# Kernel tuning notes

Measured on AMD Instinct MI355X. Metric: run time of the kernel, lower is better.

## Reference

```python
import jax, jax.numpy as jnp
import numpy as np

WINDOW = 5
PAD = WINDOW // 2


def _extract_patches(x):
    # x: (B,C,H,W) -> patches (B,C,K*K,H,W) with reflect padding, matching
    # F.pad(mode='reflect') + F.unfold(window, padding=0).
    B, C, H, W = x.shape
    xp = jnp.pad(x, ((0, 0), (0, 0), (PAD, PAD), (PAD, PAD)), mode='reflect')
    patches = jnp.stack(
        [xp[:, :, i:i + H, j:j + W] for i in range(WINDOW) for j in range(WINDOW)],
        axis=2,
    )
    return patches


def setup_inputs() -> dict:
    key = jax.random.key(0)
    k1, k2, k3 = jax.random.split(key, 3)
    x = jax.random.normal(k1, (4, 32, 256, 256), dtype=jnp.float32)
    mix = jax.random.normal(k2, (1, 32, 1, 1), dtype=jnp.float32)
    beta_raw = jax.random.normal(k3, (), dtype=jnp.float32)
    return {"x": x, "mix": mix, "beta_raw": beta_raw}


def reference(x, mix, beta_raw):
    patches = _extract_patches(x)  # (B,C,25,H,W)

    # Max filter (= max_pool2d over reflect-padded input, stride 1)
    max_out = jnp.max(patches, axis=2)

    # Soft (differentiable) median filter
    beta = 5.0 + 45.0 * jax.nn.sigmoid(beta_raw)
    center = jnp.mean(patches, axis=2, keepdims=True)
    weights = jax.nn.softmax(-beta * jnp.abs(patches - center), axis=2)
    median_out = jnp.sum(weights * patches, axis=2)

    lambda_c = jax.nn.sigmoid(mix)  # (1,C,1,1)
    return lambda_c * median_out + (1.0 - lambda_c) * max_out
```

## Files before the change

kernel.cpp:

```cpp
#include <hip/hip_runtime.h>
#include <math.h>

#define HW 256
#define TW 128
#define TH 32
#define LW 132
#define LH 36

__device__ __forceinline__ int reflect_idx(int i) {
    i = (i < 0) ? -i : i;
    i = (i >= HW) ? (2 * HW - 2 - i) : i;
    return i;
}

__device__ __forceinline__ float4 max4(float4 a, float4 b) {
    float4 r; r.x = fmaxf(a.x, b.x); r.y = fmaxf(a.y, b.y);
    r.z = fmaxf(a.z, b.z); r.w = fmaxf(a.w, b.w); return r;
}
__device__ __forceinline__ float4 add4(float4 a, float4 b) {
    float4 r; r.x = a.x + b.x; r.y = a.y + b.y;
    r.z = a.z + b.z; r.w = a.w + b.w; return r;
}
__device__ __forceinline__ float4 sub4(float4 a, float4 b) {
    float4 r; r.x = a.x - b.x; r.y = a.y - b.y;
    r.z = a.z - b.z; r.w = a.w - b.w; return r;
}

#define PROC_ROW(A0,B0,A1,B1,A2,B2,A3,B3,A4,B4, OUTROW)                         \
  do {                                                                          \
    const float4 cmA = max4(max4(max4(A0,A1), max4(A2,A3)), A4);                \
    const float4 cmB = max4(max4(max4(B0,B1), max4(B2,B3)), B4);                \
    const float csv[8] = {csA.x,csA.y,csA.z,csA.w, csB.x,csB.y,csB.z,csB.w};    \
    const float cmv[8] = {cmA.x,cmA.y,cmA.z,cmA.w, cmB.x,cmB.y,cmB.z,cmB.w};    \
    const float vv[5][8] = {                                                    \
      {A0.x,A0.y,A0.z,A0.w, B0.x,B0.y,B0.z,B0.w},                               \
      {A1.x,A1.y,A1.z,A1.w, B1.x,B1.y,B1.z,B1.w},                               \
      {A2.x,A2.y,A2.z,A2.w, B2.x,B2.y,B2.z,B2.w},                               \
      {A3.x,A3.y,A3.z,A3.w, B3.x,B3.y,B3.z,B3.w},                               \
      {A4.x,A4.y,A4.z,A4.w, B4.x,B4.y,B4.z,B4.w}};                              \
    float o[4];                                                                 \
    _Pragma("unroll")                                                           \
    for (int p = 0; p < 4; ++p) {                                               \
      const float sum  = csv[p]+csv[p+1]+csv[p+2]+csv[p+3]+csv[p+4];            \
      const float mean = sum * 0.04f;                                           \
      const float m = fmaxf(fmaxf(fmaxf(cmv[p],cmv[p+1]),                       \
                                  fmaxf(cmv[p+2],cmv[p+3])), cmv[p+4]);         \
      float wsum = 0.0f, wacc = 0.0f;                                           \
      _Pragma("unroll")                                                         \
      for (int k = 0; k < 5; ++k) {                                             \
        _Pragma("unroll")                                                       \
        for (int j = 0; j < 5; ++j) {                                           \
          const float d = vv[k][p+j] - mean;                                    \
          const float e = __builtin_amdgcn_exp2f(fabsf(d) * nbl2e);             \
          wsum += e;                                                            \
          wacc = fmaf(e, d, wacc);                                              \
        }                                                                       \
      }                                                                         \
      const float med = fmaf(wacc, __builtin_amdgcn_rcpf(wsum), mean);          \
      o[p] = fmaf(lam, med - m, m);                                             \
    }                                                                           \
    float4 o4; o4.x = o[0]; o4.y = o[1]; o4.z = o[2]; o4.w = o[3];              \
    *(float4*)(orow + (size_t)(OUTROW) * HW) = o4;                              \
  } while (0)

__global__ __launch_bounds__(256, 4)
void maxmedian_kernel(const float* __restrict__ x,
                      const float* __restrict__ mix,
                      const float* __restrict__ beta_raw,
                      float* __restrict__ out,
                      int C) {
    __shared__ __align__(16) float tile[LH * LW];

    const int tiles_x = HW / TW;
    const int tiles_per_plane = tiles_x * (HW / TH);
    const int plane = blockIdx.x / tiles_per_plane;
    const int t     = blockIdx.x % tiles_per_plane;
    const int ty0 = (t / tiles_x) * TH;
    const int tx0 = (t % tiles_x) * TW;

    const float* __restrict__ xp = x + (size_t)plane * (HW * HW);
    const int tid = threadIdx.x;

    {
        const int c  = tid & 127;
        const int r0 = tid >> 7;
        const int gx = tx0 + c;
        #pragma unroll
        for (int k = 0; k < 18; ++k) {
            const int r  = r0 + 2 * k;
            const int gy = reflect_idx(ty0 + r - 2);
            tile[r * LW + (c + 2)] = xp[gy * HW + gx];
        }
        if (tid < 144) {
            const int jj = tid & 3;
            const int j  = (jj < 2) ? jj : (128 + jj);
            const int r  = tid >> 2;
            const int gx2 = reflect_idx(tx0 + j - 2);
            const int gy2 = reflect_idx(ty0 + r - 2);
            tile[r * LW + j] = xp[gy2 * HW + gx2];
        }
    }
    __syncthreads();

    const int ch = plane % C;
    const float lam  = 1.0f / (1.0f + __expf(-mix[ch]));
    const float beta = 5.0f + 45.0f / (1.0f + __expf(-beta_raw[0]));
    const float nbl2e = -beta * 1.44269504088896f;

    const int tx  = tid & 31;
    const int tyq = tid >> 5;
    const int r0 = tyq * 4;

    const float* lbase = &tile[r0 * LW + 4 * tx];

    float4 w0a = *(const float4*)(lbase + 0 * LW);
    float4 w0b = *(const float4*)(lbase + 0 * LW + 4);
    float4 w1a = *(const float4*)(lbase + 1 * LW);
    float4 w1b = *(const float4*)(lbase + 1 * LW + 4);
    float4 w2a = *(const float4*)(lbase + 2 * LW);
    float4 w2b = *(const float4*)(lbase + 2 * LW + 4);
    float4 w3a = *(const float4*)(lbase + 3 * LW);
    float4 w3b = *(const float4*)(lbase + 3 * LW + 4);
    float4 w4a = *(const float4*)(lbase + 4 * LW);
    float4 w4b = *(const float4*)(lbase + 4 * LW + 4);

    float4 csA = add4(add4(add4(w0a, w1a), add4(w2a, w3a)), w4a);
    float4 csB = add4(add4(add4(w0b, w1b), add4(w2b, w3b)), w4b);

    float* __restrict__ orow =
        out + (size_t)plane * (HW * HW) + (size_t)(ty0 + r0) * HW + (tx0 + 4 * tx);

    PROC_ROW(w0a,w0b, w1a,w1b, w2a,w2b, w3a,w3b, w4a,w4b, 0);
    {
        const float4 na = *(const float4*)(lbase + 5 * LW);
        const float4 nb = *(const float4*)(lbase + 5 * LW + 4);
        csA = add4(csA, sub4(na, w0a));
        csB = add4(csB, sub4(nb, w0b));
        w0a = na; w0b = nb;
    }
    PROC_ROW(w1a,w1b, w2a,w2b, w3a,w3b, w4a,w4b, w0a,w0b, 1);
    {
        const float4 na = *(const float4*)(lbase + 6 * LW);
        const float4 nb = *(const float4*)(lbase + 6 * LW + 4);
        csA = add4(csA, sub4(na, w1a));
        csB = add4(csB, sub4(nb, w1b));
        w1a = na; w1b = nb;
    }
    PROC_ROW(w2a,w2b, w3a,w3b, w4a,w4b, w0a,w0b, w1a,w1b, 2);
    {
        const float4 na = *(const float4*)(lbase + 7 * LW);
        const float4 nb = *(const float4*)(lbase + 7 * LW + 4);
        csA = add4(csA, sub4(na, w2a));
        csB = add4(csB, sub4(nb, w2b));
        w2a = na; w2b = nb;
    }
    PROC_ROW(w3a,w3b, w4a,w4b, w0a,w0b, w1a,w1b, w2a,w2b, 3);
}

extern "C" void kernel_launch(void* const* d_in, const int* in_sizes, int n_in,
                              void* d_out, int out_size, void* d_ws, size_t ws_size,
                              hipStream_t stream) {
    const float* x        = (const float*)d_in[0];
    const float* mix      = (const float*)d_in[1];
    const float* beta_raw = (const float*)d_in[2];
    float* out            = (float*)d_out;

    const int planes = in_sizes[0] / (HW * HW);
    const int C      = in_sizes[1];
    const int tiles_per_plane = (HW / TW) * (HW / TH);
    const int grid = planes * tiles_per_plane;

    maxmedian_kernel<<<grid, 256, 0, stream>>>(x, mix, beta_raw, out, C);
}
```

Measured before the change: 45.78 us.

## Halve tile width, process two rows per thread, and pre-scale exp arguments by beta

Tile width drops from 128 to 64, so there are twice as many blocks, and each thread now computes 2 output rows instead of 4. The per-pixel math pre-multiplies by beta*log2e, which turns each exp argument into a single fma followed by a negated abs. Horizontal window sums and maxes share partial sums across the 4 pixels, and vertical column maxes are shared between the two rows. The aim is more parallelism and fewer ALU ops per exp, at the cost of more halo overhead per output and less vertical reuse of the sliding window.

After: 39.57 us. 13.6% less time.

```diff
diff --git a/kernel.cpp b/kernel.cpp
--- a/kernel.cpp
+++ b/kernel.cpp
@@ -2,9 +2,9 @@
 #include <math.h>
 
 #define HW 256
-#define TW 128
+#define TW 64
 #define TH 32
-#define LW 132
+#define LW 68
 #define LH 36
 
 __device__ __forceinline__ int reflect_idx(int i) {
@@ -17,6 +17,10 @@
     float4 r; r.x = fmaxf(a.x, b.x); r.y = fmaxf(a.y, b.y);
     r.z = fmaxf(a.z, b.z); r.w = fmaxf(a.w, b.w); return r;
 }
+__device__ __forceinline__ float4 max34(float4 a, float4 b, float4 c) {
+    float4 r; r.x = fmaxf(fmaxf(a.x, b.x), c.x); r.y = fmaxf(fmaxf(a.y, b.y), c.y);
+    r.z = fmaxf(fmaxf(a.z, b.z), c.z); r.w = fmaxf(fmaxf(a.w, b.w), c.w); return r;
+}
 __device__ __forceinline__ float4 add4(float4 a, float4 b) {
     float4 r; r.x = a.x + b.x; r.y = a.y + b.y;
     r.z = a.z + b.z; r.w = a.w + b.w; return r;
@@ -26,42 +30,66 @@
     r.z = a.z - b.z; r.w = a.w - b.w; return r;
 }
 
-#define PROC_ROW(A0,B0,A1,B1,A2,B2,A3,B3,A4,B4, OUTROW)                         \
-  do {                                                                          \
-    const float4 cmA = max4(max4(max4(A0,A1), max4(A2,A3)), A4);                \
-    const float4 cmB = max4(max4(max4(B0,B1), max4(B2,B3)), B4);                \
-    const float csv[8] = {csA.x,csA.y,csA.z,csA.w, csB.x,csB.y,csB.z,csB.w};    \
-    const float cmv[8] = {cmA.x,cmA.y,cmA.z,cmA.w, cmB.x,cmB.y,cmB.z,cmB.w};    \
-    const float vv[5][8] = {                                                    \
-      {A0.x,A0.y,A0.z,A0.w, B0.x,B0.y,B0.z,B0.w},                               \
-      {A1.x,A1.y,A1.z,A1.w, B1.x,B1.y,B1.z,B1.w},                               \
-      {A2.x,A2.y,A2.z,A2.w, B2.x,B2.y,B2.z,B2.w},                               \
-      {A3.x,A3.y,A3.z,A3.w, B3.x,B3.y,B3.z,B3.w},                               \
-      {A4.x,A4.y,A4.z,A4.w, B4.x,B4.y,B4.z,B4.w}};                              \
-    float o[4];                                                                 \
-    _Pragma("unroll")                                                           \
-    for (int p = 0; p < 4; ++p) {                                               \
-      const float sum  = csv[p]+csv[p+1]+csv[p+2]+csv[p+3]+csv[p+4];            \
-      const float mean = sum * 0.04f;                                           \
-      const float m = fmaxf(fmaxf(fmaxf(cmv[p],cmv[p+1]),                       \
-                                  fmaxf(cmv[p+2],cmv[p+3])), cmv[p+4]);         \
-      float wsum = 0.0f, wacc = 0.0f;                                           \
-      _Pragma("unroll")                                                         \
-      for (int k = 0; k < 5; ++k) {                                             \
-        _Pragma("unroll")                                                       \
-        for (int j = 0; j < 5; ++j) {                                           \
-          const float d = vv[k][p+j] - mean;                                    \
-          const float e = __builtin_amdgcn_exp2f(fabsf(d) * nbl2e);             \
-          wsum += e;                                                            \
-          wacc = fmaf(e, d, wacc);                                              \
-        }                                                                       \
-      }                                                                         \
-      const float med = fmaf(wacc, __builtin_amdgcn_rcpf(wsum), mean);          \
-      o[p] = fmaf(lam, med - m, m);                                             \
-    }                                                                           \
-    float4 o4; o4.x = o[0]; o4.y = o[1]; o4.z = o[2]; o4.w = o[3];              \
-    *(float4*)(orow + (size_t)(OUTROW) * HW) = o4;                              \
-  } while (0)
+__device__ __forceinline__ void proc_row(
+    float4 A0, float4 B0, float4 A1, float4 B1, float4 A2, float4 B2,
+    float4 A3, float4 B3, float4 A4, float4 B4,
+    float4 cmA, float4 cmB, float4 csA, float4 csB,
+    float bp, float c04b, float inv_bp, float lam,
+    float* __restrict__ orow)
+{
+    const float cs[8] = {csA.x,csA.y,csA.z,csA.w, csB.x,csB.y,csB.z,csB.w};
+    const float cm[8] = {cmA.x,cmA.y,cmA.z,cmA.w, cmB.x,cmB.y,cmB.z,cmB.w};
+    const float vv[5][8] = {
+        {A0.x,A0.y,A0.z,A0.w, B0.x,B0.y,B0.z,B0.w},
+        {A1.x,A1.y,A1.z,A1.w, B1.x,B1.y,B1.z,B1.w},
+        {A2.x,A2.y,A2.z,A2.w, B2.x,B2.y,B2.z,B2.w},
+        {A3.x,A3.y,A3.z,A3.w, B3.x,B3.y,B3.z,B3.w},
+        {A4.x,A4.y,A4.z,A4.w, B4.x,B4.y,B4.z,B4.w}};
+
+    const float t12 = cs[1] + cs[2];
+    const float t34 = cs[3] + cs[4];
+    const float t56 = cs[5] + cs[6];
+    const float u   = t12 + t34;
+    const float w_  = t34 + t56;
+    const float S[4] = {cs[0] + u, u + cs[5], cs[2] + w_, w_ + cs[7]};
+
+    const float h12 = fmaxf(cm[1], cm[2]);
+    const float h34 = fmaxf(cm[3], cm[4]);
+    const float h56 = fmaxf(cm[5], cm[6]);
+    const float m[4] = {fmaxf(fmaxf(cm[0], h12), h34),
+                        fmaxf(fmaxf(h12, h34), cm[5]),
+                        fmaxf(fmaxf(cm[2], h34), h56),
+                        fmaxf(fmaxf(h34, h56), cm[7])};
+
+    float bm[4], ws[4], wa[4];
+    #pragma unroll
+    for (int p = 0; p < 4; ++p) { bm[p] = S[p] * c04b; ws[p] = 0.0f; wa[p] = 0.0f; }
+
+    #pragma unroll
+    for (int k = 0; k < 5; ++k) {
+        #pragma unroll
+        for (int j = 0; j < 5; ++j) {
+            #pragma unroll
+            for (int p = 0; p < 4; ++p) {
+                const float tv = fmaf(bp, vv[k][p + j], -bm[p]);
+                const float e  = __builtin_amdgcn_exp2f(-fabsf(tv));
+                ws[p] += e;
+                wa[p] = fmaf(e, tv, wa[p]);
+            }
+        }
+    }
+
+    float4 o4;
+    float o[4];
+    #pragma unroll
+    for (int p = 0; p < 4; ++p) {
+        const float mean = S[p] * 0.04f;
+        const float med  = fmaf(wa[p] * __builtin_amdgcn_rcpf(ws[p]), inv_bp, mean);
+        o[p] = fmaf(lam, med - m[p], m[p]);
+    }
+    o4.x = o[0]; o4.y = o[1]; o4.z = o[2]; o4.w = o[3];
+    *(float4*)orow = o4;
+}
 
 __global__ __launch_bounds__(256, 4)
 void maxmedian_kernel(const float* __restrict__ x,
@@ -82,18 +110,18 @@
     const int tid = threadIdx.x;
 
     {
-        const int c  = tid & 127;
-        const int r0 = tid >> 7;
-        const int gx = tx0 + c;
+        const int c   = tid & 63;
+        const int r0s = tid >> 6;
+        const int gx  = tx0 + c;
         #pragma unroll
-        for (int k = 0; k < 18; ++k) {
-            const int r  = r0 + 2 * k;
+        for (int k = 0; k < 9; ++k) {
+            const int r  = r0s + 4 * k;
             const int gy = reflect_idx(ty0 + r - 2);
-            tile[r * LW + (c + 2)] = xp[gy * HW + gx];
+            tile[r * LW + c + 2] = xp[gy * HW + gx];
         }
         if (tid < 144) {
             const int jj = tid & 3;
-            const int j  = (jj < 2) ? jj : (128 + jj);
+            const int j  = (jj < 2) ? jj : (64 + jj);
             const int r  = tid >> 2;
             const int gx2 = reflect_idx(tx0 + j - 2);
             const int gy2 = reflect_idx(ty0 + r - 2);
@@ -105,12 +133,13 @@
     const int ch = plane % C;
     const float lam  = 1.0f / (1.0f + __expf(-mix[ch]));
     const float beta = 5.0f + 45.0f / (1.0f + __expf(-beta_raw[0]));
-    const float nbl2e = -beta * 1.44269504088896f;
+    const float bp     = beta * 1.44269504088896f;
+    const float inv_bp = 1.0f / bp;
+    const float c04b   = 0.04f * bp;
 
-    const int tx  = tid & 31;
-    const int tyq = tid >> 5;
-    const int r0 = tyq * 4;
-
+    const int tx  = tid & 15;
+    const int ryq = tid >> 4;
+    const int r0  = ryq * 2;
     const float* lbase = &tile[r0 * LW + 4 * tx];
 
     float4 w0a = *(const float4*)(lbase + 0 * LW);
@@ -123,38 +152,30 @@
     float4 w3b = *(const float4*)(lbase + 3 * LW + 4);
     float4 w4a = *(const float4*)(lbase + 4 * LW);
     float4 w4b = *(const float4*)(lbase + 4 * LW + 4);
+    float4 w5a = *(const float4*)(lbase + 5 * LW);
+    float4 w5b = *(const float4*)(lbase + 5 * LW + 4);
 
     float4 csA = add4(add4(add4(w0a, w1a), add4(w2a, w3a)), w4a);
     float4 csB = add4(add4(add4(w0b, w1b), add4(w2b, w3b)), w4b);
 
+    const float4 p12a = max4(w1a, w2a), p12b = max4(w1b, w2b);
+    const float4 p34a = max4(w3a, w4a), p34b = max4(w3b, w4b);
+    const float4 cm0a = max34(w0a, p12a, p34a);
+    const float4 cm0b = max34(w0b, p12b, p34b);
+
     float* __restrict__ orow =
         out + (size_t)plane * (HW * HW) + (size_t)(ty0 + r0) * HW + (tx0 + 4 * tx);
 
-    PROC_ROW(w0a,w0b, w1a,w1b, w2a,w2b, w3a,w3b, w4a,w4b, 0);
-    {
-        const float4 na = *(const float4*)(lbase + 5 * LW);
-        const float4 nb = *(const float4*)(lbase + 5 * LW + 4);
-        csA = add4(csA, sub4(na, w0a));
-        csB = add4(csB, sub4(nb, w0b));
-        w0a = na; w0b = nb;
-    }
-    PROC_ROW(w1a,w1b, w2a,w2b, w3a,w3b, w4a,w4b, w0a,w0b, 1);
-    {
-        const float4 na = *(const float4*)(lbase + 6 * LW);
-        const float4 nb = *(const float4*)(lbase + 6 * LW + 4);
-        csA = add4(csA, sub4(na, w1a));
-        csB = add4(csB, sub4(nb, w1b));
-        w1a = na; w1b = nb;
-    }
-    PROC_ROW(w2a,w2b, w3a,w3b, w4a,w4b, w0a,w0b, w1a,w1b, 2);
-    {
-        const float4 na = *(const float4*)(lbase + 7 * LW);
-        const float4 nb = *(const float4*)(lbase + 7 * LW + 4);
-        csA = add4(csA, sub4(na, w2a));
-        csB = add4(csB, sub4(nb, w2b));
-        w2a = na; w2b = nb;
-    }
-    PROC_ROW(w3a,w3b, w4a,w4b, w0a,w0b, w1a,w1b, w2a,w2b, 3);
+    proc_row(w0a,w0b, w1a,w1b, w2a,w2b, w3a,w3b, w4a,w4b,
+             cm0a, cm0b, csA, csB, bp, c04b, inv_bp, lam, orow);
+
+    csA = add4(csA, sub4(w5a, w0a));
+    csB = add4(csB, sub4(w5b, w0b));
+    const float4 cm1a = max34(p12a, p34a, w5a);
+    const float4 cm1b = max34(p12b, p34b, w5b);
+
+    proc_row(w1a,w1b, w2a,w2b, w3a,w3b, w4a,w4b, w5a,w5b,
+             cm1a, cm1b, csA, csB, bp, c04b, inv_bp, lam, orow + HW);
 }
 
 extern "C" void kernel_launch(void* const* d_in, const int* in_sizes, int n_in,
```
